# Kernel optimization log

Measured on AMD Instinct MI355X. Metric: run time of the kernel, lower is better.

Reference implementation:

```python
import jax, jax.numpy as jnp
import numpy as np

NUM_LEVELS = 4
SEARCH_RADIUS = 4
EPS = 1e-12  # torch F.normalize eps


def _avg_pool2d(x, s):
    # avg pool with kernel=stride=s over last two dims (exact, since H,W divisible by s)
    lead = x.shape[:-2]
    H, W = x.shape[-2], x.shape[-1]
    x = x.reshape(*lead, H // s, s, W // s, s)
    return x.mean(axis=(-3, -1))


def _l2_normalize(x, axis):
    n = jnp.sqrt(jnp.sum(x * x, axis=axis, keepdims=True))
    return x / jnp.maximum(n, EPS)


def _compute_correlation(query, values, radius):
    # query: [B,C,H,W], values: [B,N,C,H,W] -> [B,N,H,W,(2r+1)^2]
    q = _l2_normalize(query, axis=1)
    v = _l2_normalize(values, axis=2)
    corrs = []
    for dy in range(-radius, radius + 1):
        for dx in range(-radius, radius + 1):
            vs = v if (dy == 0 and dx == 0) else jnp.roll(v, (dy, dx), axis=(-2, -1))
            corrs.append(jnp.einsum('bchw,bnchw->bnhw', q, vs))
    return jnp.stack(corrs, axis=-1)


def setup_inputs() -> dict:
    key = jax.random.key(0)
    k1, k2, k3, k4 = jax.random.split(key, 4)
    B, N, C, H, W = 2, 4, 128, 160, 160
    Co = C // 2
    return {
        'query_feat': jax.random.normal(k1, (B, C, H, W), dtype=jnp.float32),
        'value_feats': jax.random.normal(k2, (B, N, C, H, W), dtype=jnp.float32),
        'proj_w': jax.random.normal(k3, (Co, C), dtype=jnp.float32) * (1.0 / np.sqrt(C)),
        'proj_b': jax.random.normal(k4, (Co,), dtype=jnp.float32) * 0.01,
    }


def reference(query_feat, value_feats, proj_w, proj_b):
    # 1x1 conv projection C -> C//2
    q = jnp.einsum('oc,bchw->bohw', proj_w, query_feat) + proj_b[None, :, None, None]
    v = jnp.einsum('oc,bnchw->bnohw', proj_w, value_feats) + proj_b[None, None, :, None, None]
    outs = []
    for level in range(NUM_LEVELS):
        scale = 2 ** level
        radius = max(1, SEARCH_RADIUS // scale)
        if scale > 1:
            q_l = _avg_pool2d(q, scale)
            v_l = _avg_pool2d(v, scale)
        else:
            q_l, v_l = q, v
        outs.append(_compute_correlation(q_l, v_l, radius))
    return tuple(outs)
```

## Files before the change

kernel.cpp:

```cpp
#include <hip/hip_runtime.h>


typedef _Float16 f16;
typedef _Float16 f16x4 __attribute__((ext_vector_type(4)));
typedef _Float16 f16x8 __attribute__((ext_vector_type(8)));
typedef float f32x4 __attribute__((ext_vector_type(4)));

#define EPSN 1e-12f

#define XS 136

__global__ __launch_bounds__(256, 3) void proj_mfma(
    const float* __restrict__ xq, const float* __restrict__ xv,
    const float* __restrict__ wt, const float* __restrict__ bias,
    float* __restrict__ outf, f16* __restrict__ outh, int P) {
  __shared__ f16 xs[128 * XS];
  __shared__ f16 ws[64 * XS];

  int bid = blockIdx.x;
  int img = bid / 200;
  int p0 = (bid - img * 200) * 128;
  const float* xsrc = (img < 2) ? (xq + (size_t)img * 128 * P)
                                : (xv + (size_t)(img - 2) * 128 * P);

  int tid = threadIdx.x;
  int lane = tid & 63;
  int wv = tid >> 6;
  int cl = lane & 15;
  int quad = lane >> 4;

  for (int it = tid; it < 64 * 16; it += 256) {
    int o = it >> 4, g = it & 15;
    float4 w0 = *(const float4*)(wt + o * 128 + g * 8);
    float4 w1 = *(const float4*)(wt + o * 128 + g * 8 + 4);
    f16x8 h;
    h[0] = (f16)w0.x; h[1] = (f16)w0.y; h[2] = (f16)w0.z; h[3] = (f16)w0.w;
    h[4] = (f16)w1.x; h[5] = (f16)w1.y; h[6] = (f16)w1.z; h[7] = (f16)w1.w;
    *(f16x8*)(ws + o * XS + g * 8) = h;
  }

  {
    int pxs = tid & 127;
    int c0 = (tid >> 7) * 64;
    const float* xp = xsrc + (size_t)c0 * P + p0 + pxs;
#pragma unroll
    for (int i = 0; i < 8; ++i) {
      float v[8];
#pragma unroll
      for (int k = 0; k < 8; ++k) v[k] = xp[(size_t)(8 * i + k) * P];
      f16x8 h;
#pragma unroll
      for (int k = 0; k < 8; ++k) h[k] = (f16)v[k];
      *(f16x8*)(xs + pxs * XS + c0 + 8 * i) = h;
    }
  }
  __syncthreads();

  f32x4 acc[2][4];
#pragma unroll
  for (int a = 0; a < 2; ++a)
#pragma unroll
    for (int m = 0; m < 4; ++m) acc[a][m] = (f32x4)0.f;

#pragma unroll
  for (int kc = 0; kc < 4; ++kc) {
    f16x8 bfr[2], afr[4];
#pragma unroll
    for (int pt = 0; pt < 2; ++pt) {
      int px = (2 * wv + pt) * 16 + cl;
      bfr[pt] = *(const f16x8*)(xs + px * XS + kc * 32 + quad * 8);
    }
#pragma unroll
    for (int mt = 0; mt < 4; ++mt) {
      int o = mt * 16 + cl;
      afr[mt] = *(const f16x8*)(ws + o * XS + kc * 32 + quad * 8);
    }
#pragma unroll
    for (int pt = 0; pt < 2; ++pt)
#pragma unroll
      for (int mt = 0; mt < 4; ++mt)
        acc[pt][mt] = __builtin_amdgcn_mfma_f32_16x16x32_f16(afr[mt], bfr[pt], acc[pt][mt], 0, 0, 0);
  }

  float4 bi[4];
#pragma unroll
  for (int mt = 0; mt < 4; ++mt) bi[mt] = *(const float4*)(bias + mt * 16 + quad * 4);

#pragma unroll
  for (int pt = 0; pt < 2; ++pt) {
    int px = p0 + (2 * wv + pt) * 16 + cl;
    float ss = 0.f;
#pragma unroll
    for (int mt = 0; mt < 4; ++mt) {
      acc[pt][mt][0] += bi[mt].x;
      acc[pt][mt][1] += bi[mt].y;
      acc[pt][mt][2] += bi[mt].z;
      acc[pt][mt][3] += bi[mt].w;
#pragma unroll
      for (int r = 0; r < 4; ++r) ss = fmaf(acc[pt][mt][r], acc[pt][mt][r], ss);
    }
    ss += __shfl_xor(ss, 16, 64);
    ss += __shfl_xor(ss, 32, 64);
    float s = 1.0f / fmaxf(sqrtf(ss), EPSN);
    size_t base = ((size_t)img * P + px) * 64;
#pragma unroll
    for (int mt = 0; mt < 4; ++mt) {
      *(float4*)(outf + base + mt * 16 + quad * 4) =
          make_float4(acc[pt][mt][0], acc[pt][mt][1], acc[pt][mt][2], acc[pt][mt][3]);
      f16x4 hn;
      hn[0] = (f16)(acc[pt][mt][0] * s);
      hn[1] = (f16)(acc[pt][mt][1] * s);
      hn[2] = (f16)(acc[pt][mt][2] * s);
      hn[3] = (f16)(acc[pt][mt][3] * s);
      *(f16x4*)(outh + base + mt * 16 + quad * 4) = hn;
    }
  }
}

__global__ __launch_bounds__(256) void pool_kernel(
    const float* __restrict__ in, float* __restrict__ out,
    int Hi, int Wi, int total) {
  int gid = blockIdx.x * 256 + threadIdx.x;
  if (gid >= total) return;
  int Ho = Hi >> 1, Wo = Wi >> 1;
  int c4 = gid & 15;
  int rest = gid >> 4;
  int wo = rest % Wo; rest /= Wo;
  int ho = rest % Ho;
  int img = rest / Ho;
  const float4* in4 = (const float4*)in;
  size_t i00 = (((size_t)img * Hi + 2 * ho) * Wi + 2 * wo) * 16 + c4;
  float4 a = in4[i00];
  float4 b = in4[i00 + 16];
  float4 c = in4[i00 + (size_t)Wi * 16];
  float4 d = in4[i00 + (size_t)Wi * 16 + 16];
  float4 r;
  r.x = 0.25f * (a.x + b.x + c.x + d.x);
  r.y = 0.25f * (a.y + b.y + c.y + d.y);
  r.z = 0.25f * (a.z + b.z + c.z + d.z);
  r.w = 0.25f * (a.w + b.w + c.w + d.w);
  ((float4*)out)[gid] = r;
}

__global__ __launch_bounds__(256) void norm16_kernel(
    const float* __restrict__ in, f16* __restrict__ out, int npix) {
  int gid = blockIdx.x * 256 + threadIdx.x;
  if (gid >= npix) return;
  const float4* p = (const float4*)in + (size_t)gid * 16;
  float4 v[16];
  float ss = 0.f;
#pragma unroll
  for (int i = 0; i < 16; ++i) {
    v[i] = p[i];
    ss = fmaf(v[i].x, v[i].x, ss);
    ss = fmaf(v[i].y, v[i].y, ss);
    ss = fmaf(v[i].z, v[i].z, ss);
    ss = fmaf(v[i].w, v[i].w, ss);
  }
  float s = 1.0f / fmaxf(sqrtf(ss), EPSN);
  f16x8* o8 = (f16x8*)(out + (size_t)gid * 64);
#pragma unroll
  for (int i = 0; i < 8; ++i) {
    float4 a = v[2 * i], b = v[2 * i + 1];
    f16x8 h;
    h[0] = (f16)(a.x * s); h[1] = (f16)(a.y * s);
    h[2] = (f16)(a.z * s); h[3] = (f16)(a.w * s);
    h[4] = (f16)(b.x * s); h[5] = (f16)(b.y * s);
    h[6] = (f16)(b.z * s); h[7] = (f16)(b.w * s);
    o8[i] = h;
  }
}

template <int R>
__global__ __launch_bounds__(256, 8) void corr_mfma(
    const f16* __restrict__ qh, const f16* __restrict__ vh,
    float* __restrict__ out, int H, int W, int T) {
  constexpr int D = 2 * R + 1, DD = D * D;
  int bn = blockIdx.x & 7;
  int wv = threadIdx.x >> 6;
  int widx = (blockIdx.x >> 3) * 4 + wv;
  int h = widx / T;
  int wt = widx - h * T;
  int lane = threadIdx.x & 63;
  int cl = lane & 15, quad = lane >> 4;
  int b = bn >> 2;
  int w0 = wt * 16;

  int ap = w0 + cl; if (ap >= W) ap = W - 1;
  const f16* qp = qh + ((size_t)(b * H + h) * W + ap) * 64 + quad * 8;
  f16x8 a0 = *(const f16x8*)qp;
  f16x8 a1 = *(const f16x8*)(qp + 32);

  int c0 = w0 - R + cl; if (c0 < 0) c0 += W; if (c0 >= W) c0 -= W;
  int c1 = w0 + R + cl; if (c1 >= W) c1 -= W;
  int b0off = c0 * 64 + quad * 8;
  int b1off = c1 * 64 + quad * 8;

  int rbase = quad * 4;
  int base_dxi = rbase - cl + ((quad < 2) ? 2 * R : 0);
  int wr0 = w0 + rbase;
  int off0 = ((bn * H + h) * W + wr0) * DD + base_dxi;

  for (int dyi = 0; dyi < D; ++dyi) {
    int h2 = h - dyi + R; if (h2 < 0) h2 += H; else if (h2 >= H) h2 -= H;
    const f16* vrow = vh + ((size_t)(bn * H + h2) * W) * 64;
    f16x8 b0a = *(const f16x8*)(vrow + b0off);
    f16x8 b0b = *(const f16x8*)(vrow + b0off + 32);
    f16x8 b1a = *(const f16x8*)(vrow + b1off);
    f16x8 b1b = *(const f16x8*)(vrow + b1off + 32);
    f32x4 A0 = __builtin_amdgcn_mfma_f32_16x16x32_f16(a0, b0a, (f32x4)0.f, 0, 0, 0);
    A0 = __builtin_amdgcn_mfma_f32_16x16x32_f16(a1, b0b, A0, 0, 0, 0);
    f32x4 A1 = __builtin_amdgcn_mfma_f32_16x16x32_f16(a0, b1a, (f32x4)0.f, 0, 0, 0);
    A1 = __builtin_amdgcn_mfma_f32_16x16x32_f16(a1, b1b, A1, 0, 0, 0);
#pragma unroll
    for (int rr = 0; rr < 4; ++rr) {
      int dxi = base_dxi + rr;
      float val = (quad < 2) ? A0[rr] : A1[rr];
      if ((unsigned)dxi <= (unsigned)(2 * R) && (wr0 + rr) < W)
        out[off0 + dyi * D + rr * (DD + 1)] = val;
    }
  }
}

extern "C" void kernel_launch(void* const* d_in, const int* in_sizes, int n_in,
                              void* d_out, int out_size, void* d_ws, size_t ws_size,
                              hipStream_t stream) {
  const float* query  = (const float*)d_in[0];
  const float* values = (const float*)d_in[1];
  const float* pw     = (const float*)d_in[2];
  const float* pb     = (const float*)d_in[3];
  float* out = (float*)d_out;
  float* ws  = (float*)d_ws;

  const int B = 2, N = 4;
  const int P0 = 160 * 160;

  float* q0 = ws;
  float* v0 = q0 + (size_t)B * P0 * 64;
  float* q1 = v0 + (size_t)B * N * P0 * 64;
  float* v1 = q1 + (size_t)B * (P0 / 4) * 64;
  float* q2 = v1 + (size_t)B * N * (P0 / 4) * 64;
  float* v2 = q2 + (size_t)B * (P0 / 16) * 64;
  float* q3 = v2 + (size_t)B * N * (P0 / 16) * 64;
  float* v3 = q3 + (size_t)B * (P0 / 64) * 64;
  float* fend = v3 + (size_t)B * N * (P0 / 64) * 64;
  f16* q0h = (f16*)fend;
  f16* v0h = q0h + (size_t)B * P0 * 64;
  f16* h13 = (f16*)ws;
  f16* qh1 = h13;
  f16* vh1 = qh1 + (size_t)B * (P0 / 4) * 64;
  f16* qh2 = vh1 + (size_t)B * N * (P0 / 4) * 64;
  f16* vh2 = qh2 + (size_t)B * (P0 / 16) * 64;
  f16* qh3 = vh2 + (size_t)B * N * (P0 / 16) * 64;
  f16* vh3 = qh3 + (size_t)B * (P0 / 64) * 64;

  proj_mfma<<<2000, 256, 0, stream>>>(query, values, pw, pb, q0, q0h, P0);

  {
    int t;
    t = 10 * (P0 / 4) * 16;   pool_kernel<<<(t + 255) / 256, 256, 0, stream>>>(q0, q1, 160, 160, t);
    t = 10 * (P0 / 16) * 16;  pool_kernel<<<(t + 255) / 256, 256, 0, stream>>>(q1, q2, 80, 80, t);
    t = 10 * (P0 / 64) * 16;  pool_kernel<<<(t + 255) / 256, 256, 0, stream>>>(q2, q3, 40, 40, t);
  }
  {
    int t = 10 * (P0 / 4 + P0 / 16 + P0 / 64);
    norm16_kernel<<<(t + 255) / 256, 256, 0, stream>>>(q1, h13, t);
  }
  float* out0 = out;
  float* out1 = out0 + (size_t)B * N * P0 * 81;
  float* out2 = out1 + (size_t)B * N * (P0 / 4) * 25;
  float* out3 = out2 + (size_t)B * N * (P0 / 16) * 9;
  corr_mfma<4><<<8 * 160 * 10 / 4, 256, 0, stream>>>(q0h, v0h, out0, 160, 160, 10);
  corr_mfma<2><<<8 * 80 * 5 / 4, 256, 0, stream>>>(qh1, vh1, out1, 80, 80, 5);
  corr_mfma<1><<<8 * 40 * 3 / 4, 256, 0, stream>>>(qh2, vh2, out2, 40, 40, 3);
  corr_mfma<1><<<8 * 20 * 2 / 4, 256, 0, stream>>>(qh3, vh3, out3, 20, 20, 2);
}
```

Baseline: 332.8 us.

## Fuse three pooling levels and normalization into one kernel; batch projection loads

Replaces three separate avg-pool launches and a normalize-to-fp16 kernel with a single kernel. Each thread loads a 4x4 block of level-0 projections, computes levels 1-3 in registers, and normalizes and writes fp16 outputs directly, using cross-lane shuffles for the channel norms and the level-3 reduction. This removes the fp32 intermediate writes and re-reads and three launches. The projection kernel also issues all 64 strided loads up front to increase memory-level parallelism, at the cost of more registers.

```diff
diff --git a/kernel.cpp b/kernel.cpp
--- a/kernel.cpp
+++ b/kernel.cpp
@@ -43,14 +43,14 @@
     int pxs = tid & 127;
     int c0 = (tid >> 7) * 64;
     const float* xp = xsrc + (size_t)c0 * P + p0 + pxs;
+    float v[64];
+#pragma unroll
+    for (int k = 0; k < 64; ++k) v[k] = xp[(size_t)k * P];
 #pragma unroll
     for (int i = 0; i < 8; ++i) {
-      float v[8];
-#pragma unroll
-      for (int k = 0; k < 8; ++k) v[k] = xp[(size_t)(8 * i + k) * P];
       f16x8 h;
 #pragma unroll
-      for (int k = 0; k < 8; ++k) h[k] = (f16)v[k];
+      for (int k = 0; k < 8; ++k) h[k] = (f16)v[8 * i + k];
       *(f16x8*)(xs + pxs * XS + c0 + 8 * i) = h;
     }
   }
@@ -117,57 +117,103 @@
   }
 }
 
-__global__ __launch_bounds__(256) void pool_kernel(
-    const float* __restrict__ in, float* __restrict__ out,
-    int Hi, int Wi, int total) {
+__global__ __launch_bounds__(256) void pool_all(
+    const float* __restrict__ q0, f16* __restrict__ qh1,
+    f16* __restrict__ qh2, f16* __restrict__ qh3) {
   int gid = blockIdx.x * 256 + threadIdx.x;
-  if (gid >= total) return;
-  int Ho = Hi >> 1, Wo = Wi >> 1;
   int c4 = gid & 15;
-  int rest = gid >> 4;
-  int wo = rest % Wo; rest /= Wo;
-  int ho = rest % Ho;
-  int img = rest / Ho;
-  const float4* in4 = (const float4*)in;
-  size_t i00 = (((size_t)img * Hi + 2 * ho) * Wi + 2 * wo) * 16 + c4;
-  float4 a = in4[i00];
-  float4 b = in4[i00 + 16];
-  float4 c = in4[i00 + (size_t)Wi * 16];
-  float4 d = in4[i00 + (size_t)Wi * 16 + 16];
-  float4 r;
-  r.x = 0.25f * (a.x + b.x + c.x + d.x);
-  r.y = 0.25f * (a.y + b.y + c.y + d.y);
-  r.z = 0.25f * (a.z + b.z + c.z + d.z);
-  r.w = 0.25f * (a.w + b.w + c.w + d.w);
-  ((float4*)out)[gid] = r;
-}
-
-__global__ __launch_bounds__(256) void norm16_kernel(
-    const float* __restrict__ in, f16* __restrict__ out, int npix) {
-  int gid = blockIdx.x * 256 + threadIdx.x;
-  if (gid >= npix) return;
-  const float4* p = (const float4*)in + (size_t)gid * 16;
-  float4 v[16];
-  float ss = 0.f;
-#pragma unroll
-  for (int i = 0; i < 16; ++i) {
-    v[i] = p[i];
-    ss = fmaf(v[i].x, v[i].x, ss);
-    ss = fmaf(v[i].y, v[i].y, ss);
-    ss = fmaf(v[i].z, v[i].z, ss);
-    ss = fmaf(v[i].w, v[i].w, ss);
-  }
-  float s = 1.0f / fmaxf(sqrtf(ss), EPSN);
-  f16x8* o8 = (f16x8*)(out + (size_t)gid * 64);
-#pragma unroll
-  for (int i = 0; i < 8; ++i) {
-    float4 a = v[2 * i], b = v[2 * i + 1];
-    f16x8 h;
-    h[0] = (f16)(a.x * s); h[1] = (f16)(a.y * s);
-    h[2] = (f16)(a.z * s); h[3] = (f16)(a.w * s);
-    h[4] = (f16)(b.x * s); h[5] = (f16)(b.y * s);
-    h[6] = (f16)(b.z * s); h[7] = (f16)(b.w * s);
-    o8[i] = h;
+  int g = (gid >> 4) & 3;
+  int idx = gid >> 6;
+  int w3 = idx % 20;
+  int t = idx / 20;
+  int h3 = t % 20;
+  int img = t / 20;
+  int h2 = 2 * h3 + (g >> 1);
+  int w2 = 2 * w3 + (g & 1);
+
+  const float4* in4 = (const float4*)q0;
+  size_t base = ((size_t)(img * 160 + 4 * h2) * 160 + 4 * w2) * 16 + c4;
+  float4 a[16];
+#pragma unroll
+  for (int i = 0; i < 4; ++i)
+#pragma unroll
+    for (int j = 0; j < 4; ++j)
+      a[i * 4 + j] = in4[base + (size_t)i * 160 * 16 + j * 16];
+
+  float4 v1[4];
+  float4 q2v = make_float4(0.f, 0.f, 0.f, 0.f);
+#pragma unroll
+  for (int i1 = 0; i1 < 2; ++i1)
+#pragma unroll
+    for (int j1 = 0; j1 < 2; ++j1) {
+      float4 s00 = a[(2 * i1) * 4 + 2 * j1];
+      float4 s01 = a[(2 * i1) * 4 + 2 * j1 + 1];
+      float4 s10 = a[(2 * i1 + 1) * 4 + 2 * j1];
+      float4 s11 = a[(2 * i1 + 1) * 4 + 2 * j1 + 1];
+      float4 r;
+      r.x = 0.25f * (s00.x + s01.x + s10.x + s11.x);
+      r.y = 0.25f * (s00.y + s01.y + s10.y + s11.y);
+      r.z = 0.25f * (s00.z + s01.z + s10.z + s11.z);
+      r.w = 0.25f * (s00.w + s01.w + s10.w + s11.w);
+      v1[i1 * 2 + j1] = r;
+      q2v.x += r.x; q2v.y += r.y; q2v.z += r.z; q2v.w += r.w;
+    }
+  q2v.x *= 0.25f; q2v.y *= 0.25f; q2v.z *= 0.25f; q2v.w *= 0.25f;
+
+#pragma unroll
+  for (int i1 = 0; i1 < 2; ++i1)
+#pragma unroll
+    for (int j1 = 0; j1 < 2; ++j1) {
+      float4 r = v1[i1 * 2 + j1];
+      float ss = fmaf(r.x, r.x, fmaf(r.y, r.y, fmaf(r.z, r.z, r.w * r.w)));
+      ss += __shfl_xor(ss, 1, 64);
+      ss += __shfl_xor(ss, 2, 64);
+      ss += __shfl_xor(ss, 4, 64);
+      ss += __shfl_xor(ss, 8, 64);
+      float s = 1.0f / fmaxf(sqrtf(ss), EPSN);
+      int y1 = 2 * h2 + i1, x1 = 2 * w2 + j1;
+      f16x4 h;
+      h[0] = (f16)(r.x * s); h[1] = (f16)(r.y * s);
+      h[2] = (f16)(r.z * s); h[3] = (f16)(r.w * s);
+      *(f16x4*)(qh1 + ((size_t)(img * 80 + y1) * 80 + x1) * 64 + c4 * 4) = h;
+    }
+
+  {
+    float ss = fmaf(q2v.x, q2v.x, fmaf(q2v.y, q2v.y, fmaf(q2v.z, q2v.z, q2v.w * q2v.w)));
+    ss += __shfl_xor(ss, 1, 64);
+    ss += __shfl_xor(ss, 2, 64);
+    ss += __shfl_xor(ss, 4, 64);
+    ss += __shfl_xor(ss, 8, 64);
+    float s = 1.0f / fmaxf(sqrtf(ss), EPSN);
+    f16x4 h;
+    h[0] = (f16)(q2v.x * s); h[1] = (f16)(q2v.y * s);
+    h[2] = (f16)(q2v.z * s); h[3] = (f16)(q2v.w * s);
+    *(f16x4*)(qh2 + ((size_t)(img * 40 + h2) * 40 + w2) * 64 + c4 * 4) = h;
+  }
+
+  {
+    float4 q3v;
+    q3v.x = q2v.x + __shfl_xor(q2v.x, 16, 64);
+    q3v.y = q2v.y + __shfl_xor(q2v.y, 16, 64);
+    q3v.z = q2v.z + __shfl_xor(q2v.z, 16, 64);
+    q3v.w = q2v.w + __shfl_xor(q2v.w, 16, 64);
+    q3v.x += __shfl_xor(q3v.x, 32, 64);
+    q3v.y += __shfl_xor(q3v.y, 32, 64);
+    q3v.z += __shfl_xor(q3v.z, 32, 64);
+    q3v.w += __shfl_xor(q3v.w, 32, 64);
+    q3v.x *= 0.25f; q3v.y *= 0.25f; q3v.z *= 0.25f; q3v.w *= 0.25f;
+    float ss = fmaf(q3v.x, q3v.x, fmaf(q3v.y, q3v.y, fmaf(q3v.z, q3v.z, q3v.w * q3v.w)));
+    ss += __shfl_xor(ss, 1, 64);
+    ss += __shfl_xor(ss, 2, 64);
+    ss += __shfl_xor(ss, 4, 64);
+    ss += __shfl_xor(ss, 8, 64);
+    float s = 1.0f / fmaxf(sqrtf(ss), EPSN);
+    if (g == 0) {
+      f16x4 h;
+      h[0] = (f16)(q3v.x * s); h[1] = (f16)(q3v.y * s);
+      h[2] = (f16)(q3v.z * s); h[3] = (f16)(q3v.w * s);
+      *(f16x4*)(qh3 + ((size_t)(img * 20 + h3) * 20 + w3) * 64 + c4 * 4) = h;
+    }
   }
 }
 
@@ -236,36 +282,19 @@
   const int P0 = 160 * 160;
 
   float* q0 = ws;
-  float* v0 = q0 + (size_t)B * P0 * 64;
-  float* q1 = v0 + (size_t)B * N * P0 * 64;
-  float* v1 = q1 + (size_t)B * (P0 / 4) * 64;
-  float* q2 = v1 + (size_t)B * N * (P0 / 4) * 64;
-  float* v2 = q2 + (size_t)B * (P0 / 16) * 64;
-  float* q3 = v2 + (size_t)B * N * (P0 / 16) * 64;
-  float* v3 = q3 + (size_t)B * (P0 / 64) * 64;
-  float* fend = v3 + (size_t)B * N * (P0 / 64) * 64;
-  f16* q0h = (f16*)fend;
-  f16* v0h = q0h + (size_t)B * P0 * 64;
-  f16* h13 = (f16*)ws;
-  f16* qh1 = h13;
-  f16* vh1 = qh1 + (size_t)B * (P0 / 4) * 64;
-  f16* qh2 = vh1 + (size_t)B * N * (P0 / 4) * 64;
-  f16* vh2 = qh2 + (size_t)B * (P0 / 16) * 64;
-  f16* qh3 = vh2 + (size_t)B * N * (P0 / 16) * 64;
-  f16* vh3 = qh3 + (size_t)B * (P0 / 64) * 64;
+  f16* q0h = (f16*)(ws + (size_t)10 * P0 * 64);
+  f16* v0h = q0h + (size_t)2 * P0 * 64;
+  f16* qh1 = q0h + (size_t)10 * P0 * 64;
+  f16* vh1 = qh1 + (size_t)2 * (P0 / 4) * 64;
+  f16* qh2 = vh1 + (size_t)8 * (P0 / 4) * 64;
+  f16* vh2 = qh2 + (size_t)2 * (P0 / 16) * 64;
+  f16* qh3 = vh2 + (size_t)8 * (P0 / 16) * 64;
+  f16* vh3 = qh3 + (size_t)2 * (P0 / 64) * 64;
 
   proj_mfma<<<2000, 256, 0, stream>>>(query, values, pw, pb, q0, q0h, P0);
 
-  {
-    int t;
-    t = 10 * (P0 / 4) * 16;   pool_kernel<<<(t + 255) / 256, 256, 0, stream>>>(q0, q1, 160, 160, t);
-    t = 10 * (P0 / 16) * 16;  pool_kernel<<<(t + 255) / 256, 256, 0, stream>>>(q1, q2, 80, 80, t);
-    t = 10 * (P0 / 64) * 16;  pool_kernel<<<(t + 255) / 256, 256, 0, stream>>>(q2, q3, 40, 40, t);
-  }
-  {
-    int t = 10 * (P0 / 4 + P0 / 16 + P0 / 64);
-    norm16_kernel<<<(t + 255) / 256, 256, 0, stream>>>(q1, h13, t);
-  }
+  pool_all<<<1000, 256, 0, stream>>>(q0, qh1, qh2, qh3);
+
   float* out0 = out;
   float* out1 = out0 + (size_t)B * N * P0 * 81;
   float* out2 = out1 + (size_t)B * N * (P0 / 4) * 25;
```

Measured after the change: 317.0 us. -4.8%, faster.
